# Optimization experiments

Hardware: AMD Instinct MI355X
Metric: run time of the kernel (lower is better)

## Reference

```python
import jax, jax.numpy as jnp
import numpy as np

B, S, H = 16, 4096, 1024   # batch, seq_len, hidden_dim
NSEG = 512                  # max segments (distinct output_mask ids) per example


def setup_inputs() -> dict:
    key = jax.random.key(0)
    k1, k2 = jax.random.split(key)
    hidden_states = jax.random.normal(k1, (B, S, H), dtype=jnp.float32)
    # non-decreasing segment ids per row, as the original loop requires
    output_mask = jnp.sort(jax.random.randint(k2, (B, S), 0, NSEG), axis=-1)
    return {"hidden_states": hidden_states, "output_mask": output_mask}


def reference(hidden_states, output_mask):
    # Fused equivalent of the per-token Python loop: mean-pool tokens sharing
    # the same (batch, segment_id) group; tokens with id == -1 are dropped.
    b, s, h = hidden_states.shape
    valid = output_mask >= 0                                     # [B, S]
    batch_idx = jnp.arange(b, dtype=output_mask.dtype)[:, None]  # [B, 1]
    # global segment id; invalid tokens routed to a dummy trailing bucket
    gid = jnp.where(valid, batch_idx * NSEG + output_mask, b * NSEG)
    gid_flat = gid.reshape(-1)                                   # [B*S]
    x = hidden_states.reshape(-1, h)                             # [B*S, H]
    sums = jax.ops.segment_sum(x, gid_flat, num_segments=b * NSEG + 1)[:-1]
    ones = jnp.ones((b * s,), dtype=hidden_states.dtype)
    counts = jax.ops.segment_sum(ones, gid_flat, num_segments=b * NSEG + 1)[:-1]
    # segment mean; empty segments yield zeros (fixed-shape analogue of torch.cat)
    return sums / jnp.maximum(counts, 1.0)[:, None]              # [B*NSEG, H]
```

## Files before the change

kernel.cpp:

```cpp
#include <hip/hip_runtime.h>

constexpr int B    = 16;
constexpr int S    = 4096;
constexpr int H    = 1024;
constexpr int NSEG = 512;

__global__ __launch_bounds__(256) void seg_bounds_kernel(
    const int* __restrict__ mask,
    int*       __restrict__ bounds)
{
    const int idx = blockIdx.x * blockDim.x + threadIdx.x;
    const int b = idx >> 12;
    const int i = idx & (S - 1);

    const int* row  = mask + b * S;
    int*       brow = bounds + b * (NSEG + 1);

    int cur  = row[i];
    int prev = (i == 0) ? -1 : row[i - 1];

    if (cur  > NSEG - 1) cur  = NSEG - 1;
    if (prev < -1)       prev = -1;

    for (int s = prev + 1; s <= cur; ++s) brow[s] = i;
    if (i == S - 1) {
        for (int s = (cur < 0 ? 0 : cur + 1); s <= NSEG; ++s) brow[s] = S;
    }
}

__global__ __launch_bounds__(256) void seg_mean_kernel(
    const float* __restrict__ hs,
    const int*   __restrict__ bounds,
    float*       __restrict__ out)
{
    const int gid = blockIdx.x;
    const int b   = gid >> 9;
    const int seg = gid & (NSEG - 1);

    const int* brow  = bounds + b * (NSEG + 1);
    const int  start = brow[seg];
    const int  end   = brow[seg + 1];
    const int  cnt   = end - start;

    const int col = threadIdx.x << 2;

    const float* base = hs + ((size_t)b * S + (size_t)start) * H + col;

    float4 a0 = make_float4(0.f, 0.f, 0.f, 0.f);
    float4 a1 = make_float4(0.f, 0.f, 0.f, 0.f);

    int t = 0;
    for (; t + 4 <= cnt; t += 4) {
        float4 v0 = *reinterpret_cast<const float4*>(base + (size_t)(t + 0) * H);
        float4 v1 = *reinterpret_cast<const float4*>(base + (size_t)(t + 1) * H);
        float4 v2 = *reinterpret_cast<const float4*>(base + (size_t)(t + 2) * H);
        float4 v3 = *reinterpret_cast<const float4*>(base + (size_t)(t + 3) * H);
        a0.x += v0.x; a0.y += v0.y; a0.z += v0.z; a0.w += v0.w;
        a1.x += v1.x; a1.y += v1.y; a1.z += v1.z; a1.w += v1.w;
        a0.x += v2.x; a0.y += v2.y; a0.z += v2.z; a0.w += v2.w;
        a1.x += v3.x; a1.y += v3.y; a1.z += v3.z; a1.w += v3.w;
    }
    for (; t < cnt; ++t) {
        float4 v = *reinterpret_cast<const float4*>(base + (size_t)t * H);
        a0.x += v.x; a0.y += v.y; a0.z += v.z; a0.w += v.w;
    }

    a0.x += a1.x; a0.y += a1.y; a0.z += a1.z; a0.w += a1.w;

    const float inv = (cnt > 0) ? (1.0f / (float)cnt) : 0.0f;
    a0.x *= inv; a0.y *= inv; a0.z *= inv; a0.w *= inv;

    *reinterpret_cast<float4*>(out + (size_t)gid * H + col) = a0;
}

extern "C" void kernel_launch(void* const* d_in, const int* in_sizes, int n_in,
                              void* d_out, int out_size, void* d_ws, size_t ws_size,
                              hipStream_t stream) {
    const float* hs   = (const float*)d_in[0];
    const int*   mask = (const int*)  d_in[1];

    float* out    = (float*)d_out;
    int*   bounds = (int*)d_ws;

    seg_bounds_kernel<<<dim3((B * S) / 256), dim3(256), 0, stream>>>(mask, bounds);
    seg_mean_kernel <<<dim3(B * NSEG),       dim3(256), 0, stream>>>(hs, bounds, out);
}
```

Measured before the change: 56.33 us.

## Fuse segment-boundary search into mean kernel via two-level wave ballot search

```diff
diff --git a/kernel.cpp b/kernel.cpp
--- a/kernel.cpp
+++ b/kernel.cpp
@@ -5,42 +5,41 @@
 constexpr int H    = 1024;
 constexpr int NSEG = 512;
 
-__global__ __launch_bounds__(256) void seg_bounds_kernel(
-    const int* __restrict__ mask,
-    int*       __restrict__ bounds)
-{
-    const int idx = blockIdx.x * blockDim.x + threadIdx.x;
-    const int b = idx >> 12;
-    const int i = idx & (S - 1);
-
-    const int* row  = mask + b * S;
-    int*       brow = bounds + b * (NSEG + 1);
-
-    int cur  = row[i];
-    int prev = (i == 0) ? -1 : row[i - 1];
-
-    if (cur  > NSEG - 1) cur  = NSEG - 1;
-    if (prev < -1)       prev = -1;
-
-    for (int s = prev + 1; s <= cur; ++s) brow[s] = i;
-    if (i == S - 1) {
-        for (int s = (cur < 0 ? 0 : cur + 1); s <= NSEG; ++s) brow[s] = S;
-    }
-}
-
-__global__ __launch_bounds__(256) void seg_mean_kernel(
+__global__ __launch_bounds__(256) void seg_mean_fused_kernel(
     const float* __restrict__ hs,
-    const int*   __restrict__ bounds,
+    const int*   __restrict__ mask,
     float*       __restrict__ out)
 {
     const int gid = blockIdx.x;
     const int b   = gid >> 9;
     const int seg = gid & (NSEG - 1);
 
-    const int* brow  = bounds + b * (NSEG + 1);
-    const int  start = brow[seg];
-    const int  end   = brow[seg + 1];
-    const int  cnt   = end - start;
+    __shared__ int s_bounds[2];
+
+    const int wave = threadIdx.x >> 6;
+    const int lane = threadIdx.x & 63;
+
+    if (wave < 2) {
+        const int  x   = seg + wave;
+        const int* row = mask + b * S;
+
+        int p1 = row[lane * 64 + 63];
+        unsigned long long m1 = __ballot(p1 >= x);
+        int bound;
+        if (m1 == 0ull) {
+            bound = S;
+        } else {
+            int c = __ffsll((unsigned long long)m1) - 1;
+            int p2 = row[c * 64 + lane];
+            unsigned long long m2 = __ballot(p2 >= x);
+            bound = c * 64 + (__ffsll((unsigned long long)m2) - 1);
+        }
+        if (lane == 0) s_bounds[wave] = bound;
+    }
+    __syncthreads();
+
+    const int start = s_bounds[0];
+    const int cnt   = s_bounds[1] - start;
 
     const int col = threadIdx.x << 2;
 
@@ -79,9 +78,7 @@
     const float* hs   = (const float*)d_in[0];
     const int*   mask = (const int*)  d_in[1];
 
-    float* out    = (float*)d_out;
-    int*   bounds = (int*)d_ws;
+    float* out = (float*)d_out;
 
-    seg_bounds_kernel<<<dim3((B * S) / 256), dim3(256), 0, stream>>>(mask, bounds);
-    seg_mean_kernel <<<dim3(B * NSEG),       dim3(256), 0, stream>>>(hs, bounds, out);
+    seg_mean_fused_kernel<<<dim3(B * NSEG), dim3(256), 0, stream>>>(hs, mask, out);
 }
```

After: 50.70 us. 10.0% less time.
